# Kernel optimization log

Measured on AMD Instinct MI355X. Metric: run time of the kernel, lower is better.

## Reference

```python
import jax, jax.numpy as jnp
import numpy as np
from jax import lax

LAYER_NUM = 6
EPS = 1e-9
BN_EPS = 1e-5

# CNOT ring on 3 qubits: CNOT(0,1), CNOT(1,2), CNOT(2,0); qubit 0 = MSB.
_P = np.zeros((8, 8), np.float32)
for _b in range(8):
    b0, b1, b2 = (_b >> 2) & 1, (_b >> 1) & 1, _b & 1
    b1 ^= b0
    b2 ^= b1
    b0 ^= b2
    _P[(b0 << 2) | (b1 << 1) | b2, _b] = 1.0
CNOT_RING = jnp.asarray(_P)


def _ry(t):
    c, s = jnp.cos(t / 2), jnp.sin(t / 2)
    return jnp.stack([jnp.stack([c, -s]), jnp.stack([s, c])])


def _channel_unitary(wc):
    # wc: [layer_num, 3] rotation angles -> full 8x8 circuit unitary (real, RY+CNOT)
    U = jnp.eye(8, dtype=wc.dtype)
    for l in range(wc.shape[0]):
        K = jnp.kron(jnp.kron(_ry(wc[l, 0]), _ry(wc[l, 1])), _ry(wc[l, 2]))
        U = CNOT_RING @ K @ U
    return U


def qcnn(x, weights, out_dim, out_size):
    # x: [B, C, H, W]; weights: [C, layer_num, 3]; 2x2 kernel, stride 2, no padding
    B, C, H, W = x.shape
    OH, OW = H // 2, W // 2
    # im2col: [B, C*4, OH, OW] with feature dim ordered (C, kh, kw)
    patches = lax.conv_general_dilated_patches(x, (2, 2), (2, 2), 'VALID')
    patches = patches.reshape(B, C, 4, OH * OW).transpose(0, 1, 3, 2)  # [B,C,P,4]
    # amplitude embedding on 2 data qubits, ancilla (MSB) in |0>
    nrm = jnp.linalg.norm(patches, axis=-1, keepdims=True)
    amp = patches / jnp.maximum(nrm, EPS)
    psi0 = jnp.pad(amp, ((0, 0), (0, 0), (0, 0), (0, 4)))  # [B,C,P,8]
    U = jax.vmap(_channel_unitary)(weights)  # [C,8,8]
    psi = jnp.einsum('cjk,bcpk->bcpj', U, psi0)
    probs = psi * psi
    data = probs[..., :4]  # post-select ancilla = 0
    data = data / jnp.maximum(data.sum(-1, keepdims=True), EPS)
    return data.reshape(B, out_dim, out_size, out_size)


def batchnorm2d(x, gamma, beta):
    mean = x.mean(axis=(0, 2, 3), keepdims=True)
    var = x.var(axis=(0, 2, 3), keepdims=True)
    xn = (x - mean) * lax.rsqrt(var + BN_EPS)
    return xn * gamma[None, :, None, None] + beta[None, :, None, None]


def setup_inputs() -> dict:
    key = jax.random.key(0)
    ks = jax.random.split(key, 5)
    return {
        'z': jax.random.normal(ks[0], (1024, 256, 4, 4), jnp.float32),
        'w1': jax.random.normal(ks[1], (256, LAYER_NUM, 3), jnp.float32),
        'w2': jax.random.normal(ks[2], (64, LAYER_NUM, 3), jnp.float32),
        'w3': jax.random.normal(ks[3], (16, LAYER_NUM, 3), jnp.float32),
        'w4': jax.random.normal(ks[4], (4, LAYER_NUM, 3), jnp.float32),
        'gamma2': jnp.ones((64,), jnp.float32), 'beta2': jnp.zeros((64,), jnp.float32),
        'gamma3': jnp.ones((16,), jnp.float32), 'beta3': jnp.zeros((16,), jnp.float32),
        'gamma4': jnp.ones((4,), jnp.float32), 'beta4': jnp.zeros((4,), jnp.float32),
        'gamma_f': jnp.ones((1,), jnp.float32), 'beta_f': jnp.zeros((1,), jnp.float32),
    }


def reference(z, w1, w2, w3, w4, gamma2, beta2, gamma3, beta3, gamma4, beta4, gamma_f, beta_f):
    s1 = qcnn(z, w1, 64, 8)
    x = jax.nn.relu(batchnorm2d(s1, gamma2, beta2))
    s2 = qcnn(x, w2, 16, 16)
    x = jax.nn.relu(batchnorm2d(s2, gamma3, beta3))
    s3 = qcnn(x, w3, 4, 32)
    x = jax.nn.relu(batchnorm2d(s3, gamma4, beta4))
    s4 = qcnn(x, w4, 1, 64)
    s4_bn = batchnorm2d(s4, gamma_f, beta_f)
    return jnp.tanh(s4_bn), s4, s4_bn
```

## Files before the change

### kernel.cpp

```cpp
#include <hip/hip_runtime.h>
#include <math.h>


#define NSLOT 32
#define NBLK  1024u
#define TPB   512

#define OFF_G2S 0
#define OFF_G2Q 2048
#define OFF_G3S 4096
#define OFF_G3Q 4608
#define OFF_G4S 5120
#define OFF_G4Q 5248
#define OFF_GFS 5376
#define OFF_GFQ 5408
#define OFF_CTR 5504
#define PHASE_STRIDE 2192
#define OFF_VG  16512

__device__ __forceinline__ void gbar(unsigned* ctr, int phase)
{
    __syncthreads();
    if (threadIdx.x == 0){
        unsigned* base  = ctr + phase*PHASE_STRIDE;
        const int  lf   = blockIdx.x & 63;
        unsigned* leaf  = base + (lf << 4);
        unsigned* mid   = base + 1024 + ((lf >> 3) << 4);
        unsigned* root  = base + 1152;
        unsigned* flags = base + 1168;

        unsigned ol = __hip_atomic_fetch_add(leaf, 1u, __ATOMIC_RELAXED,
                                             __HIP_MEMORY_SCOPE_AGENT);
        if (ol == 15u){
            unsigned om = __hip_atomic_fetch_add(mid, 1u, __ATOMIC_RELAXED,
                                                 __HIP_MEMORY_SCOPE_AGENT);
            if (om == 7u){
                unsigned orr = __hip_atomic_fetch_add(root, 1u, __ATOMIC_RELAXED,
                                                      __HIP_MEMORY_SCOPE_AGENT);
                if (orr == 7u){
                    #pragma unroll
                    for (int i=0;i<64;i++)
                        __hip_atomic_store(flags + (i<<4), 1u, __ATOMIC_RELAXED,
                                           __HIP_MEMORY_SCOPE_AGENT);
                }
            }
        }
        unsigned* myflag = flags + (lf << 4);
        int spins = 0;
        while (__hip_atomic_load(myflag, __ATOMIC_RELAXED,
                                 __HIP_MEMORY_SCOPE_AGENT) == 0u){
            __builtin_amdgcn_s_sleep(2);
            if (++spins > 200000) break;
        }
        __atomic_signal_fence(__ATOMIC_SEQ_CST);
    }
    __syncthreads();
}

__device__ __forceinline__ float llc_load(const float* p)
{
    return __hip_atomic_load(const_cast<float*>(p), __ATOMIC_RELAXED,
                             __HIP_MEMORY_SCOPE_AGENT);
}
__device__ __forceinline__ void llc_store(float* p, float v)
{
    __hip_atomic_store(p, v, __ATOMIC_RELAXED, __HIP_MEMORY_SCOPE_AGENT);
}

template<int C, int H, int W, bool BN>
__device__ __forceinline__ void qcnn_phase(
    const float* __restrict__ x, const float* __restrict__ Vg,
    const float* __restrict__ isum, const float* __restrict__ issq,
    const float* __restrict__ gamma, const float* __restrict__ beta,
    float invNin,
    float* __restrict__ out, float* __restrict__ osum, float* __restrict__ ossq,
    float* sBin, float* sV, float* sRed)
{
    constexpr int HW  = H*W;
    constexpr int P   = HW/4;
    constexpr int OW  = W/2;
    constexpr int LP  = (P==4)?2:(P==16)?4:(P==64)?6:8;
    constexpr int LOW = (OW==2)?1:(OW==4)?2:(OW==8)?3:4;
    constexpr int CPB = TPB/P;
    constexpr int OCB = (TPB/(4*P)) < 1 ? 1 : (TPB/(4*P));
    constexpr int G   = (4*P < 64) ? 4*P : 64;

    const int c0 = (blockIdx.x & 1) * CPB;

    for (int i = threadIdx.x; i < CPB*16; i += TPB)
        sV[i] = llc_load(Vg + c0*16 + i);
    if (threadIdx.x < 2*OCB) sBin[threadIdx.x] = 0.0f;
    if constexpr (BN){ if (threadIdx.x < 2*CPB) sRed[threadIdx.x] = 0.0f; }
    __syncthreads();

    if constexpr (BN){
        constexpr int TOT = 2*CPB*NSLOT;
        for (int i=threadIdx.x; i<TOT; i+=TPB){
            const int arr  = i / (CPB*NSLOT);
            const int rem  = i - arr*(CPB*NSLOT);
            const int cl   = rem >> 5;
            const int slot = rem & 31;
            float v = llc_load((arr ? issq : isum) + (c0+cl)*NSLOT + slot);
            atomicAdd(&sRed[arr*CPB + cl], v);
        }
        __syncthreads();
    }

    const int r   = ((blockIdx.x & 1) << 9) + threadIdx.x;
    const int c   = r >> LP;
    const int p   = r & (P-1);
    const int oh  = p >> LOW;
    const int ow  = p & (OW-1);
    const int oc0 = ((blockIdx.x & 1) << 9) >> (LP+2);
    const int ocl = (r >> (LP+2)) - oc0;
    const int xoff = c*HW + (oh*2)*W + (ow*2);
    const int ooff = c*HW + (p<<2);

    float sc = 0.0f, sh = 0.0f;
    if constexpr (BN){
        const int cl = c - c0;
        float s = sRed[cl], q = sRed[CPB+cl];
        float mean = s * invNin;
        float var  = q * invNin - mean*mean;
        float rinv = 1.0f / sqrtf(var + 1e-5f);
        sc = gamma[c] * rinv;
        sh = beta[c] - mean * sc;
    }
    const float4* Vc = reinterpret_cast<const float4*>(sV + (c-c0)*16);
    const float4 v0 = Vc[0], v1 = Vc[1], v2 = Vc[2], v3 = Vc[3];

    float lsA = 0.0f, lssA = 0.0f;
    #pragma unroll
    for (int it=0; it<2; ++it){
        const int b = (it<<9) + (blockIdx.x>>1);
        const float* xb = x + ((size_t)b<<12) + xoff;
        float2 t0 = *reinterpret_cast<const float2*>(xb);
        float2 t1 = *reinterpret_cast<const float2*>(xb + W);
        float x0=t0.x, x1=t0.y, x2=t1.x, x3=t1.y;
        if constexpr (BN){
            x0 = fmaxf(x0*sc+sh, 0.0f);
            x1 = fmaxf(x1*sc+sh, 0.0f);
            x2 = fmaxf(x2*sc+sh, 0.0f);
            x3 = fmaxf(x3*sc+sh, 0.0f);
        }
        float nsq = x0*x0 + x1*x1 + x2*x2 + x3*x3;
        float q0 = v0.x*x0 + v0.y*x1 + v0.z*x2 + v0.w*x3;
        float q1 = v1.x*x0 + v1.y*x1 + v1.z*x2 + v1.w*x3;
        float q2 = v2.x*x0 + v2.y*x1 + v2.z*x2 + v2.w*x3;
        float q3 = v3.x*x0 + v3.y*x1 + v3.z*x2 + v3.w*x3;
        q0*=q0; q1*=q1; q2*=q2; q3*=q3;
        float s = q0+q1+q2+q3;
        float dinv = 1.0f / fmaxf(s, 1e-9f * fmaxf(nsq, 1e-18f));
        float d0=q0*dinv, d1=q1*dinv, d2=q2*dinv, d3=q3*dinv;
        *reinterpret_cast<float4*>(out + ((size_t)b<<12) + ooff) =
            make_float4(d0,d1,d2,d3);
        lsA  += d0+d1+d2+d3;
        lssA += d0*d0 + d1*d1 + d2*d2 + d3*d3;
    }
    #pragma unroll
    for (int off=1; off<G; off<<=1){ lsA += __shfl_xor(lsA, off); lssA += __shfl_xor(lssA, off); }
    if ((threadIdx.x & (G-1)) == 0){
        atomicAdd(&sBin[ocl], lsA);
        atomicAdd(&sBin[OCB + ocl], lssA);
    }
    __syncthreads();
    if (threadIdx.x < OCB){
        const int slot = (blockIdx.x >> 1) & (NSLOT-1);
        atomicAdd(&osum[(oc0+threadIdx.x)*NSLOT + slot], sBin[threadIdx.x]);
        atomicAdd(&ossq[(oc0+threadIdx.x)*NSLOT + slot], sBin[OCB+threadIdx.x]);
    }
}

__global__ __launch_bounds__(TPB, 8) void fused_all(
    const float* __restrict__ z,
    const float* __restrict__ w1, const float* __restrict__ w2,
    const float* __restrict__ w3, const float* __restrict__ w4,
    const float* __restrict__ gamma2, const float* __restrict__ beta2,
    const float* __restrict__ gamma3, const float* __restrict__ beta3,
    const float* __restrict__ gamma4, const float* __restrict__ beta4,
    const float* __restrict__ gammaf, const float* __restrict__ betaf,
    float* __restrict__ out, float* __restrict__ ws)
{
    __shared__ float sBin[64];
    __shared__ float sV[2048];
    __shared__ float sRed[64];
    unsigned* ctr = reinterpret_cast<unsigned*>(ws + OFF_CTR);
    float* Vg   = ws + OFF_VG;
    float* bufA = ws + 65536;
    float* bufB = bufA + 4194304;
    float* s4   = out + 4194304;
    float* s4bn = out + 8388608;
    const int gtid = blockIdx.x*TPB + threadIdx.x;

    {
        const int t = blockIdx.x*2 + threadIdx.x;
        if (threadIdx.x < 2 && t < 1360){
            const int ch = t >> 2, k = t & 3;
            const float* w;
            if (ch < 256)      w = w1 + ch*18;
            else if (ch < 320) w = w2 + (ch-256)*18;
            else if (ch < 336) w = w3 + (ch-320)*18;
            else               w = w4 + (ch-336)*18;
            float v[8];
            #pragma unroll
            for (int r=0;r<8;r++) v[r] = (r==k) ? 1.0f : 0.0f;
            for (int l=0;l<6;l++){
                float ca = cosf(0.5f*w[l*3+0]), sa = sinf(0.5f*w[l*3+0]);
                float cb = cosf(0.5f*w[l*3+1]), sb = sinf(0.5f*w[l*3+1]);
                float cc = cosf(0.5f*w[l*3+2]), sc_ = sinf(0.5f*w[l*3+2]);
                #pragma unroll
                for (int b=0;b<8;b+=2){ float xx=v[b], yy=v[b+1]; v[b]=cc*xx-sc_*yy; v[b+1]=sc_*xx+cc*yy; }
                #pragma unroll
                for (int g=0; g<8; g+=4)
                    #pragma unroll
                    for (int i=0;i<2;i++){ int a=g+i, b=g+i+2; float xx=v[a], yy=v[b]; v[a]=cb*xx-sb*yy; v[b]=sb*xx+cb*yy; }
                #pragma unroll
                for (int i=0;i<4;i++){ float xx=v[i], yy=v[i+4]; v[i]=ca*xx-sa*yy; v[i+4]=sa*xx+ca*yy; }
                float nv[8];
                nv[0]=v[0]; nv[5]=v[1]; nv[7]=v[2]; nv[2]=v[3];
                nv[3]=v[4]; nv[6]=v[5]; nv[4]=v[6]; nv[1]=v[7];
                #pragma unroll
                for (int r=0;r<8;r++) v[r]=nv[r];
            }
            #pragma unroll
            for (int r=0;r<4;r++) llc_store(Vg + ch*16 + r*4 + k, v[r]);
        }
    }
    gbar(ctr, 0);

    qcnn_phase<256,4,4,false>(z, Vg, nullptr, nullptr, nullptr, nullptr, 0.0f,
                              bufA, ws+OFF_G2S, ws+OFF_G2Q, sBin, sV, sRed);
    gbar(ctr, 1);

    qcnn_phase<64,8,8,true>(bufA, Vg+256*16, ws+OFF_G2S, ws+OFF_G2Q, gamma2, beta2,
                            1.0f/65536.0f, bufB, ws+OFF_G3S, ws+OFF_G3Q, sBin, sV, sRed);
    gbar(ctr, 2);

    qcnn_phase<16,16,16,true>(bufB, Vg+320*16, ws+OFF_G3S, ws+OFF_G3Q, gamma3, beta3,
                              1.0f/262144.0f, bufA, ws+OFF_G4S, ws+OFF_G4Q, sBin, sV, sRed);
    gbar(ctr, 3);

    qcnn_phase<4,32,32,true>(bufA, Vg+336*16, ws+OFF_G4S, ws+OFF_G4Q, gamma4, beta4,
                             1.0f/1048576.0f, s4, ws+OFF_GFS, ws+OFF_GFQ, sBin, sV, sRed);
    gbar(ctr, 4);

    {
        float v = 0.0f;
        if (threadIdx.x < 64)
            v = llc_load(ws + (threadIdx.x < 32 ? OFF_GFS + threadIdx.x
                                                : OFF_GFQ + threadIdx.x - 32));
        #pragma unroll
        for (int off=1; off<32; off<<=1) v += __shfl_xor(v, off);
        if (threadIdx.x == 0)  sRed[0] = v;
        if (threadIdx.x == 32) sRed[1] = v;
        __syncthreads();
        float s = sRed[0], q = sRed[1];
        float mean = s * (1.0f/4194304.0f);
        float var  = q * (1.0f/4194304.0f) - mean*mean;
        float rinv = 1.0f / sqrtf(var + 1e-5f);
        float sc = gammaf[0]*rinv;
        float sh = betaf[0] - mean*sc;
        #pragma unroll
        for (int k=0; k<2; ++k){
            int i = gtid + k*524288;
            float4 vv = reinterpret_cast<const float4*>(s4)[i];
            float4 bn = make_float4(vv.x*sc+sh, vv.y*sc+sh, vv.z*sc+sh, vv.w*sc+sh);
            reinterpret_cast<float4*>(s4bn)[i] = bn;
            reinterpret_cast<float4*>(out)[i] =
                make_float4(tanhf(bn.x), tanhf(bn.y), tanhf(bn.z), tanhf(bn.w));
        }
    }
}

extern "C" void kernel_launch(void* const* d_in, const int* in_sizes, int n_in,
                              void* d_out, int out_size, void* d_ws, size_t ws_size,
                              hipStream_t stream)
{
    const float* z      = (const float*)d_in[0];
    const float* w1     = (const float*)d_in[1];
    const float* w2     = (const float*)d_in[2];
    const float* w3     = (const float*)d_in[3];
    const float* w4     = (const float*)d_in[4];
    const float* gamma2 = (const float*)d_in[5];
    const float* beta2  = (const float*)d_in[6];
    const float* gamma3 = (const float*)d_in[7];
    const float* beta3  = (const float*)d_in[8];
    const float* gamma4 = (const float*)d_in[9];
    const float* beta4  = (const float*)d_in[10];
    const float* gammaf = (const float*)d_in[11];
    const float* betaf  = (const float*)d_in[12];
    float* out = (float*)d_out;
    float* ws  = (float*)d_ws;

    hipMemsetAsync(ws, 0, (5504 + 5*PHASE_STRIDE) * sizeof(float), stream);

    fused_all<<<NBLK, TPB, 0, stream>>>(
        z, w1, w2, w3, w4, gamma2, beta2, gamma3, beta3,
        gamma4, beta4, gammaf, betaf, out, ws);
}
```

Baseline: 174.0 us.

## Keep inter-layer activations in shared memory instead of global buffers

Each block always handles the same half-image slice across all four QCNN layers, so each layer's outputs are written to a 16KB shared buffer and read back from there by the next layer. This removes the global round-trips through the workspace buffers between phases. Only the final layer still writes s4 to global, and the last BN/tanh pass reads from shared memory. The cost is more LDS per block, which may cut occupancy, plus an extra __syncthreads per phase.

```diff
diff --git a/kernel.cpp b/kernel.cpp
--- a/kernel.cpp
+++ b/kernel.cpp
@@ -67,14 +67,14 @@
     __hip_atomic_store(p, v, __ATOMIC_RELAXED, __HIP_MEMORY_SCOPE_AGENT);
 }
 
-template<int C, int H, int W, bool BN>
+template<int C, int H, int W, bool BN, bool FIRST, bool WG>
 __device__ __forceinline__ void qcnn_phase(
-    const float* __restrict__ x, const float* __restrict__ Vg,
+    const float* __restrict__ xg, const float* __restrict__ Vg,
     const float* __restrict__ isum, const float* __restrict__ issq,
     const float* __restrict__ gamma, const float* __restrict__ beta,
-    float invNin,
-    float* __restrict__ out, float* __restrict__ osum, float* __restrict__ ossq,
-    float* sBin, float* sV, float* sRed)
+    float invNin, float* __restrict__ outg,
+    float* __restrict__ osum, float* __restrict__ ossq,
+    float* sBin, float* sV, float* sRed, float* sX)
 {
     constexpr int HW  = H*W;
     constexpr int P   = HW/4;
@@ -85,7 +85,8 @@
     constexpr int OCB = (TPB/(4*P)) < 1 ? 1 : (TPB/(4*P));
     constexpr int G   = (4*P < 64) ? 4*P : 64;
 
-    const int c0 = (blockIdx.x & 1) * CPB;
+    const int w  = blockIdx.x & 1;
+    const int c0 = w * CPB;
 
     for (int i = threadIdx.x; i < CPB*16; i += TPB)
         sV[i] = llc_load(Vg + c0*16 + i);
@@ -106,19 +107,18 @@
         __syncthreads();
     }
 
-    const int r   = ((blockIdx.x & 1) << 9) + threadIdx.x;
+    const int r   = (w << 9) + threadIdx.x;
     const int c   = r >> LP;
     const int p   = r & (P-1);
     const int oh  = p >> LOW;
     const int ow  = p & (OW-1);
-    const int oc0 = ((blockIdx.x & 1) << 9) >> (LP+2);
+    const int oc0 = (w << 9) >> (LP+2);
     const int ocl = (r >> (LP+2)) - oc0;
-    const int xoff = c*HW + (oh*2)*W + (ow*2);
-    const int ooff = c*HW + (p<<2);
+    const int cl  = c - c0;
+    const int xl  = cl*HW + (oh*2)*W + ow*2;
 
     float sc = 0.0f, sh = 0.0f;
     if constexpr (BN){
-        const int cl = c - c0;
         float s = sRed[cl], q = sRed[CPB+cl];
         float mean = s * invNin;
         float var  = q * invNin - mean*mean;
@@ -126,17 +126,30 @@
         sc = gamma[c] * rinv;
         sh = beta[c] - mean * sc;
     }
-    const float4* Vc = reinterpret_cast<const float4*>(sV + (c-c0)*16);
+    const float4* Vc = reinterpret_cast<const float4*>(sV + cl*16);
     const float4 v0 = Vc[0], v1 = Vc[1], v2 = Vc[2], v3 = Vc[3];
+
+    float xi[2][4];
+    #pragma unroll
+    for (int it=0; it<2; ++it){
+        if constexpr (FIRST){
+            const int b = (it<<9) + (int)(blockIdx.x>>1);
+            const float* xb = xg + ((size_t)b<<12) + c*HW + (oh*2)*W + ow*2;
+            float2 t0 = *reinterpret_cast<const float2*>(xb);
+            float2 t1 = *reinterpret_cast<const float2*>(xb + W);
+            xi[it][0]=t0.x; xi[it][1]=t0.y; xi[it][2]=t1.x; xi[it][3]=t1.y;
+        } else {
+            float2 t0 = *reinterpret_cast<const float2*>(&sX[it*2048 + xl]);
+            float2 t1 = *reinterpret_cast<const float2*>(&sX[it*2048 + xl + W]);
+            xi[it][0]=t0.x; xi[it][1]=t0.y; xi[it][2]=t1.x; xi[it][3]=t1.y;
+        }
+    }
+    if constexpr (!FIRST) __syncthreads();
 
     float lsA = 0.0f, lssA = 0.0f;
     #pragma unroll
     for (int it=0; it<2; ++it){
-        const int b = (it<<9) + (blockIdx.x>>1);
-        const float* xb = x + ((size_t)b<<12) + xoff;
-        float2 t0 = *reinterpret_cast<const float2*>(xb);
-        float2 t1 = *reinterpret_cast<const float2*>(xb + W);
-        float x0=t0.x, x1=t0.y, x2=t1.x, x3=t1.y;
+        float x0=xi[it][0], x1=xi[it][1], x2=xi[it][2], x3=xi[it][3];
         if constexpr (BN){
             x0 = fmaxf(x0*sc+sh, 0.0f);
             x1 = fmaxf(x1*sc+sh, 0.0f);
@@ -152,8 +165,13 @@
         float s = q0+q1+q2+q3;
         float dinv = 1.0f / fmaxf(s, 1e-9f * fmaxf(nsq, 1e-18f));
         float d0=q0*dinv, d1=q1*dinv, d2=q2*dinv, d3=q3*dinv;
-        *reinterpret_cast<float4*>(out + ((size_t)b<<12) + ooff) =
+        *reinterpret_cast<float4*>(&sX[it*2048 + 4*threadIdx.x]) =
             make_float4(d0,d1,d2,d3);
+        if constexpr (WG){
+            const int b = (it<<9) + (int)(blockIdx.x>>1);
+            *reinterpret_cast<float4*>(outg + ((size_t)b<<12) + (w<<11)
+                                       + 4*threadIdx.x) = make_float4(d0,d1,d2,d3);
+        }
         lsA  += d0+d1+d2+d3;
         lssA += d0*d0 + d1*d1 + d2*d2 + d3*d3;
     }
@@ -184,30 +202,29 @@
     __shared__ float sBin[64];
     __shared__ float sV[2048];
     __shared__ float sRed[64];
+    __shared__ float sX[4096];
     unsigned* ctr = reinterpret_cast<unsigned*>(ws + OFF_CTR);
     float* Vg   = ws + OFF_VG;
-    float* bufA = ws + 65536;
-    float* bufB = bufA + 4194304;
     float* s4   = out + 4194304;
     float* s4bn = out + 8388608;
-    const int gtid = blockIdx.x*TPB + threadIdx.x;
+    const int w = blockIdx.x & 1;
 
     {
         const int t = blockIdx.x*2 + threadIdx.x;
         if (threadIdx.x < 2 && t < 1360){
             const int ch = t >> 2, k = t & 3;
-            const float* w;
-            if (ch < 256)      w = w1 + ch*18;
-            else if (ch < 320) w = w2 + (ch-256)*18;
-            else if (ch < 336) w = w3 + (ch-320)*18;
-            else               w = w4 + (ch-336)*18;
+            const float* wp;
+            if (ch < 256)      wp = w1 + ch*18;
+            else if (ch < 320) wp = w2 + (ch-256)*18;
+            else if (ch < 336) wp = w3 + (ch-320)*18;
+            else               wp = w4 + (ch-336)*18;
             float v[8];
             #pragma unroll
             for (int r=0;r<8;r++) v[r] = (r==k) ? 1.0f : 0.0f;
             for (int l=0;l<6;l++){
-                float ca = cosf(0.5f*w[l*3+0]), sa = sinf(0.5f*w[l*3+0]);
-                float cb = cosf(0.5f*w[l*3+1]), sb = sinf(0.5f*w[l*3+1]);
-                float cc = cosf(0.5f*w[l*3+2]), sc_ = sinf(0.5f*w[l*3+2]);
+                float ca = cosf(0.5f*wp[l*3+0]), sa = sinf(0.5f*wp[l*3+0]);
+                float cb = cosf(0.5f*wp[l*3+1]), sb = sinf(0.5f*wp[l*3+1]);
+                float cc = cosf(0.5f*wp[l*3+2]), sc_ = sinf(0.5f*wp[l*3+2]);
                 #pragma unroll
                 for (int b=0;b<8;b+=2){ float xx=v[b], yy=v[b+1]; v[b]=cc*xx-sc_*yy; v[b+1]=sc_*xx+cc*yy; }
                 #pragma unroll
@@ -228,20 +245,20 @@
     }
     gbar(ctr, 0);
 
-    qcnn_phase<256,4,4,false>(z, Vg, nullptr, nullptr, nullptr, nullptr, 0.0f,
-                              bufA, ws+OFF_G2S, ws+OFF_G2Q, sBin, sV, sRed);
+    qcnn_phase<256,4,4,false,true,false>(z, Vg, nullptr, nullptr, nullptr, nullptr,
+        0.0f, nullptr, ws+OFF_G2S, ws+OFF_G2Q, sBin, sV, sRed, sX);
     gbar(ctr, 1);
 
-    qcnn_phase<64,8,8,true>(bufA, Vg+256*16, ws+OFF_G2S, ws+OFF_G2Q, gamma2, beta2,
-                            1.0f/65536.0f, bufB, ws+OFF_G3S, ws+OFF_G3Q, sBin, sV, sRed);
+    qcnn_phase<64,8,8,true,false,false>(nullptr, Vg+256*16, ws+OFF_G2S, ws+OFF_G2Q,
+        gamma2, beta2, 1.0f/65536.0f, nullptr, ws+OFF_G3S, ws+OFF_G3Q, sBin, sV, sRed, sX);
     gbar(ctr, 2);
 
-    qcnn_phase<16,16,16,true>(bufB, Vg+320*16, ws+OFF_G3S, ws+OFF_G3Q, gamma3, beta3,
-                              1.0f/262144.0f, bufA, ws+OFF_G4S, ws+OFF_G4Q, sBin, sV, sRed);
+    qcnn_phase<16,16,16,true,false,false>(nullptr, Vg+320*16, ws+OFF_G3S, ws+OFF_G3Q,
+        gamma3, beta3, 1.0f/262144.0f, nullptr, ws+OFF_G4S, ws+OFF_G4Q, sBin, sV, sRed, sX);
     gbar(ctr, 3);
 
-    qcnn_phase<4,32,32,true>(bufA, Vg+336*16, ws+OFF_G4S, ws+OFF_G4Q, gamma4, beta4,
-                             1.0f/1048576.0f, s4, ws+OFF_GFS, ws+OFF_GFQ, sBin, sV, sRed);
+    qcnn_phase<4,32,32,true,false,true>(nullptr, Vg+336*16, ws+OFF_G4S, ws+OFF_G4Q,
+        gamma4, beta4, 1.0f/1048576.0f, s4, ws+OFF_GFS, ws+OFF_GFQ, sBin, sV, sRed, sX);
     gbar(ctr, 4);
 
     {
@@ -261,12 +278,13 @@
         float sc = gammaf[0]*rinv;
         float sh = betaf[0] - mean*sc;
         #pragma unroll
-        for (int k=0; k<2; ++k){
-            int i = gtid + k*524288;
-            float4 vv = reinterpret_cast<const float4*>(s4)[i];
+        for (int it=0; it<2; ++it){
+            const int b = (it<<9) + (int)(blockIdx.x>>1);
+            const size_t go = ((size_t)b<<12) + (w<<11) + 4*threadIdx.x;
+            float4 vv = *reinterpret_cast<const float4*>(&sX[it*2048 + 4*threadIdx.x]);
             float4 bn = make_float4(vv.x*sc+sh, vv.y*sc+sh, vv.z*sc+sh, vv.w*sc+sh);
-            reinterpret_cast<float4*>(s4bn)[i] = bn;
-            reinterpret_cast<float4*>(out)[i] =
+            *reinterpret_cast<float4*>(s4bn + go) = bn;
+            *reinterpret_cast<float4*>(out + go) =
                 make_float4(tanhf(bn.x), tanhf(bn.y), tanhf(bn.z), tanhf(bn.w));
         }
     }
```

New measurement: 170.9 us. About the same (-1.8%).
